# Kernel optimization log

Measured on AMD Instinct MI355X. Metric: run time of the kernel, lower is better.

Reference implementation:

```python
import jax, jax.numpy as jnp
import numpy as np
import math

D, DK, DV = 1024, 128, 128
B, S = 4, 2048

def setup_inputs() -> dict:
    key = jax.random.key(0)
    k1, k2, k3, k4 = jax.random.split(key, 4)
    # xavier_normal std = sqrt(2/(fan_in+fan_out))
    std_qk = math.sqrt(2.0 / (D + DK))
    std_v = math.sqrt(2.0 / (D + DV))
    return {
        "X": jax.random.normal(k1, (B, S, D), dtype=jnp.float32),
        "W_q": jax.random.normal(k2, (D, DK), dtype=jnp.float32) * std_qk,
        "W_k": jax.random.normal(k3, (D, DK), dtype=jnp.float32) * std_qk,
        "W_v": jax.random.normal(k4, (D, DV), dtype=jnp.float32) * std_v,
    }

def reference(X, W_q, W_k, W_v):
    # Q,K,V projections: [B,S,D] @ [D,dk] -> [B,S,dk]
    Q = X @ W_q
    K = X @ W_k
    V = X @ W_v
    scale = 1.0 / math.sqrt(DK)
    # NOTE: original torch code calls A.masked_fill(...) without assigning the
    # result, so the causal mask is never actually applied. We replicate the
    # executed math: unmasked scaled dot-product attention.
    A = jnp.einsum("bqd,bkd->bqk", Q, K) * scale  # [B,S,S]
    A = jax.nn.softmax(A, axis=2)
    return jnp.einsum("bqk,bkv->bqv", A, V)  # [B,S,DV]
```

## Files before the change

kernel.cpp:

```cpp
#include <hip/hip_runtime.h>
#include <stdint.h>
#include <math.h>


typedef __attribute__((ext_vector_type(4))) float  f32x4;
typedef __attribute__((ext_vector_type(4))) short  s16x4;
typedef __attribute__((ext_vector_type(8))) short  s16x8;
typedef __attribute__((ext_vector_type(4))) float  fl4;

#define MFMA16(a,b,c) __builtin_amdgcn_mfma_f32_16x16x16bf16_1k(a,b,c,0,0,0)
#define MFMA32(a,b,c) __builtin_amdgcn_mfma_f32_16x16x32_bf16(a,b,c,0,0,0)

__device__ __forceinline__ short f2bf(float f){
  uint32_t u = __builtin_bit_cast(uint32_t, f);
  u = (u + 0x7FFFu + ((u >> 16) & 1u)) >> 16;
  return (short)u;
}

#define S_LEN   2048
#define D_IN    1024
#define D_HEAD  128
#define NROWS   8192
#define NSPLIT  8
#define KVB     64
#define KVPER   (S_LEN / NSPLIT)
#define NT      (KVPER / KVB)
#define QBLK    64

#define WT_OFF  0u
#define Q_OFF   786432u
#define K_OFF   (786432u + 2097152u)
#define V_OFF   (786432u + 2u*2097152u)
#define OP_OFF  (786432u + 3u*2097152u)
#define ML_OFF  (OP_OFF + 33554432u)

#define LOG2E   1.4426950408889634f
#define DEFER_TH 11.541560327111708f

__global__ __launch_bounds__(256) void wt3_kernel(
    const float* __restrict__ Wq, const float* __restrict__ Wk,
    const float* __restrict__ Wv, short* __restrict__ Wt){
  int i = blockIdx.x * 256 + threadIdx.x;
  int m = i >> 17;
  int r = i & 131071;
  int n = r >> 10;
  int k = r & 1023;
  const float* W = (m == 0) ? Wq : (m == 1 ? Wk : Wv);
  float v = W[k * D_HEAD + n];
  if (m == 0) v *= 0.08838834764831845f * LOG2E;
  Wt[i] = f2bf(v);
}

__global__ __launch_bounds__(256) void proj_kernel(
    const float* __restrict__ X, const short* __restrict__ Wt,
    short* __restrict__ Qo, short* __restrict__ Ko, short* __restrict__ Vt){
  const int mt  = blockIdx.x;
  const int mat = blockIdx.y;
  const short* Wm = Wt + mat * 131072;

  __shared__ short Xs[64][72];
  __shared__ short Ws[128][72];

  const int tid  = threadIdx.x;
  const int lane = tid & 63;
  const int wid  = tid >> 6;
  const int wm   = (wid >> 1) * 32;
  const int wn   = (wid & 1) * 64;
  const int lr   = lane & 15;
  const int lg8  = (lane >> 4) * 8;

  const f32x4 zero4 = {0.f, 0.f, 0.f, 0.f};
  f32x4 acc[2][4];
  #pragma unroll
  for (int mf = 0; mf < 2; mf++)
    #pragma unroll
    for (int n = 0; n < 4; n++) acc[mf][n] = zero4;

  const int xr = tid >> 2, xc = (tid & 3) * 16;
  const int wr = tid >> 1, wc = (tid & 1) * 32;

  const float* xsrc0 = X + (size_t)(mt * 64 + xr) * D_IN + xc;
  const short* wsrc0 = Wm + (size_t)wr * D_IN + wc;

  fl4   xA[4];
  s16x8 wR[4];

  #pragma unroll
  for (int j = 0; j < 4; j++){
    xA[j] = *(const fl4*)(xsrc0 + 4 * j);
    wR[j] = *(const s16x8*)(wsrc0 + 8 * j);
  }

  #pragma unroll 1
  for (int kt = 0; kt < D_IN; kt += 64){
    {
      s16x8 v0, v1;
      #pragma unroll
      for (int j = 0; j < 4; j++){
        v0[j] = f2bf(xA[0][j]); v0[j+4] = f2bf(xA[1][j]);
        v1[j] = f2bf(xA[2][j]); v1[j+4] = f2bf(xA[3][j]);
      }
      *(s16x8*)&Xs[xr][xc]     = v0;
      *(s16x8*)&Xs[xr][xc + 8] = v1;
      #pragma unroll
      for (int j = 0; j < 4; j++) *(s16x8*)&Ws[wr][wc + 8*j] = wR[j];
    }
    __syncthreads();

    if (kt + 64 < D_IN){
      #pragma unroll
      for (int j = 0; j < 4; j++){
        xA[j] = *(const fl4*)(xsrc0 + kt + 64 + 4*j);
        wR[j] = *(const s16x8*)(wsrc0 + kt + 64 + 8*j);
      }
    }

    #pragma unroll
    for (int kc = 0; kc < 64; kc += 32){
      s16x8 af[2];
      #pragma unroll
      for (int mf = 0; mf < 2; mf++)
        af[mf] = *(const s16x8*)&Xs[wm + mf*16 + lr][kc + lg8];
      #pragma unroll
      for (int n = 0; n < 4; n++){
        s16x8 bf = *(const s16x8*)&Ws[wn + n*16 + lr][kc + lg8];
        #pragma unroll
        for (int mf = 0; mf < 2; mf++)
          acc[mf][n] = MFMA32(af[mf], bf, acc[mf][n]);
      }
    }
    __syncthreads();
  }

  const int lg4 = (lane >> 4) * 4;
  if (mat < 2){
    short* dst = (mat == 0) ? Qo : Ko;
    #pragma unroll
    for (int mf = 0; mf < 2; mf++)
      #pragma unroll
      for (int n = 0; n < 4; n++){
        int col = wn + n*16 + lr;
        #pragma unroll
        for (int r = 0; r < 4; r++){
          int row = mt*64 + wm + mf*16 + lg4 + r;
          dst[(size_t)row * D_HEAD + col] = f2bf(acc[mf][n][r]);
        }
      }
  } else {
    const int b  = (mt * 64) >> 11;
    const int s0 = (mt * 64) & 2047;
    #pragma unroll
    for (int mf = 0; mf < 2; mf++)
      #pragma unroll
      for (int n = 0; n < 4; n++){
        int dv = wn + n*16 + lr;
        int s  = s0 + wm + mf*16 + lg4;
        s16x4 v;
        #pragma unroll
        for (int r = 0; r < 4; r++) v[r] = f2bf(acc[mf][n][r]);
        *(s16x4*)&Vt[((size_t)b * D_HEAD + dv) * S_LEN + s] = v;
      }
  }
}

__global__ __launch_bounds__(256, 4) void flash_kernel(
    const short* __restrict__ Q, const short* __restrict__ K,
    const short* __restrict__ Vt, float* __restrict__ Opart,
    float* __restrict__ MLpart){
  const int sp = blockIdx.x;
  const int qt = blockIdx.y;
  const int b  = blockIdx.z;

  __shared__ short Ks[KVB][136];
  __shared__ short Vs[128][72];

  const int tid  = threadIdx.x;
  const int lane = tid & 63;
  const int w    = tid >> 6;
  const int lr   = lane & 15;
  const int lg   = lane >> 4;

  const int qrow = qt * QBLK + w * 16 + lr;
  const short* Qr = Q + (size_t)(b * S_LEN + qrow) * D_HEAD + 8 * lg;
  s16x8 qf[4];
  #pragma unroll
  for (int c = 0; c < 4; c++) qf[c] = *(const s16x8*)(Qr + c * 32);

  const f32x4 zero4 = {0.f, 0.f, 0.f, 0.f};
  f32x4 o[8];
  #pragma unroll
  for (int t = 0; t < 8; t++) o[t] = zero4;
  float m_run = -INFINITY, l_run = 0.0f;

  const short* Kb = K  + (size_t)b * S_LEN * D_HEAD;
  const short* Vb = Vt + (size_t)b * D_HEAD * S_LEN;
  const int kr = tid >> 2, kc = (tid & 3) * 32;
  const int vr = tid >> 1, vc = (tid & 1) * 32;

  s16x8 kR[4], vR[4];
  const int kv_beg = sp * KVPER;

  {
    const short* ks = Kb + (size_t)(kv_beg + kr) * D_HEAD + kc;
    const short* vs = Vb + (size_t)vr * S_LEN + kv_beg + vc;
    #pragma unroll
    for (int j = 0; j < 4; j++){
      kR[j] = *(const s16x8*)(ks + 8*j);
      vR[j] = *(const s16x8*)(vs + 8*j);
    }
  }
  #pragma unroll
  for (int j = 0; j < 4; j++){
    *(s16x8*)&Ks[kr][kc + 8*j] = kR[j];
    *(s16x8*)&Vs[vr][vc + 8*j] = vR[j];
  }
  __syncthreads();

  #pragma unroll 1
  for (int it = 0; it < NT; ++it){
    if (it + 1 < NT){
      int kv0 = kv_beg + (it + 1) * KVB;
      const short* ks = Kb + (size_t)(kv0 + kr) * D_HEAD + kc;
      const short* vs = Vb + (size_t)vr * S_LEN + kv0 + vc;
      #pragma unroll
      for (int j = 0; j < 4; j++){
        kR[j] = *(const s16x8*)(ks + 8*j);
        vR[j] = *(const s16x8*)(vs + 8*j);
      }
    }

    f32x4 sa[4];
    #pragma unroll
    for (int t = 0; t < 4; t++) sa[t] = zero4;
    __builtin_amdgcn_s_setprio(1);
    #pragma unroll
    for (int c = 0; c < 4; c++){
      #pragma unroll
      for (int t = 0; t < 4; t++){
        s16x8 ka = *(const s16x8*)&Ks[t*16 + lr][c*32 + 8*lg];
        sa[t] = MFMA32(ka, qf[c], sa[t]);
      }
    }
    __builtin_amdgcn_s_setprio(0);

    float mx = -INFINITY;
    #pragma unroll
    for (int t = 0; t < 4; t++)
      #pragma unroll
      for (int r = 0; r < 4; r++) mx = fmaxf(mx, sa[t][r]);
    mx = fmaxf(mx, __shfl_xor(mx, 16));
    mx = fmaxf(mx, __shfl_xor(mx, 32));
    if (!__all(mx <= m_run + DEFER_TH)){
      float m_new = fmaxf(m_run, mx);
      float alpha = exp2f(m_run - m_new);
      l_run *= alpha;
      #pragma unroll
      for (int t = 0; t < 8; t++) o[t] *= alpha;
      m_run = m_new;
    }
    s16x4 pb[4];
    float lsum = 0.0f;
    #pragma unroll
    for (int t = 0; t < 4; t++)
      #pragma unroll
      for (int r = 0; r < 4; r++){
        float e = exp2f(sa[t][r] - m_run);
        pb[t][r] = f2bf(e);
        lsum += e;
      }
    lsum += __shfl_xor(lsum, 16);
    lsum += __shfl_xor(lsum, 32);
    l_run += lsum;

    __builtin_amdgcn_s_setprio(1);
    #pragma unroll
    for (int dt = 0; dt < 8; dt++){
      #pragma unroll
      for (int t = 0; t < 4; t++){
        s16x4 va = *(const s16x4*)&Vs[dt*16 + lr][t*16 + 4*lg];
        o[dt] = MFMA16(va, pb[t], o[dt]);
      }
    }
    __builtin_amdgcn_s_setprio(0);

    if (it + 1 < NT){
      __syncthreads();
      #pragma unroll
      for (int j = 0; j < 4; j++){
        *(s16x8*)&Ks[kr][kc + 8*j] = kR[j];
        *(s16x8*)&Vs[vr][vc + 8*j] = vR[j];
      }
      __syncthreads();
    }
  }

  const int lg4 = lg * 4;
  const size_t grow = (size_t)b * S_LEN + qrow;
  float* Op = Opart + ((size_t)sp * NROWS + grow) * D_HEAD + lg4;
  #pragma unroll
  for (int dt = 0; dt < 8; dt++)
    *(f32x4*)(Op + dt * 16) = o[dt];
  if (lg == 0){
    float* ml = MLpart + ((size_t)sp * NROWS + grow) * 2;
    ml[0] = m_run; ml[1] = l_run;
  }
}

__global__ __launch_bounds__(256) void merge_kernel(
    const float* __restrict__ Opart, const float* __restrict__ MLpart,
    float* __restrict__ out){
  int idx = blockIdx.x * 256 + threadIdx.x;
  int row = idx >> 7;
  float m[NSPLIT], l[NSPLIT];
  float M = -INFINITY;
  #pragma unroll
  for (int s = 0; s < NSPLIT; s++){
    m[s] = MLpart[((size_t)s * NROWS + row) * 2 + 0];
    l[s] = MLpart[((size_t)s * NROWS + row) * 2 + 1];
    M = fmaxf(M, m[s]);
  }
  float L = 0.f, val = 0.f;
  #pragma unroll
  for (int s = 0; s < NSPLIT; s++){
    float e = exp2f(m[s] - M);
    L   += l[s] * e;
    val += Opart[(size_t)s * NROWS * D_HEAD + idx] * e;
  }
  out[idx] = val / L;
}

extern "C" void kernel_launch(void* const* d_in, const int* in_sizes, int n_in,
                              void* d_out, int out_size, void* d_ws, size_t ws_size,
                              hipStream_t stream){
  const float* X  = (const float*)d_in[0];
  const float* Wq = (const float*)d_in[1];
  const float* Wk = (const float*)d_in[2];
  const float* Wv = (const float*)d_in[3];
  char* ws = (char*)d_ws;
  short* Wt = (short*)(ws + WT_OFF);
  short* Qp = (short*)(ws + Q_OFF);
  short* Kp = (short*)(ws + K_OFF);
  short* Vt = (short*)(ws + V_OFF);
  float* Op = (float*)(ws + OP_OFF);
  float* Ml = (float*)(ws + ML_OFF);
  float* out = (float*)d_out;

  wt3_kernel  <<<dim3(1536),           dim3(256), 0, stream>>>(Wq, Wk, Wv, Wt);
  proj_kernel <<<dim3(128, 3),         dim3(256), 0, stream>>>(X, Wt, Qp, Kp, Vt);
  flash_kernel<<<dim3(NSPLIT, 32, 4),  dim3(256), 0, stream>>>(Qp, Kp, Vt, Op, Ml);
  merge_kernel<<<dim3(4096),           dim3(256), 0, stream>>>(Op, Ml, out);
}
```

Baseline: 129.0 us.

## Pre-convert X to bf16 and stage projection tiles via direct-to-LDS loads

The weight-transpose kernel now also converts X to bf16 into a workspace buffer, so the projection kernel no longer converts fp32 to bf16 inside its loop. The projection GEMM stages X and W tiles with global_load_lds into double-buffered shared memory using an XOR swizzle instead of padded rows, which overlaps the next tile's load with MFMA work. In exchange, all of X makes an extra round trip through memory (a 32 MB fp32 read and a 16 MB bf16 write) in the pre-pass, and the projection kernel uses more LDS.

```diff
diff --git a/kernel.cpp b/kernel.cpp
--- a/kernel.cpp
+++ b/kernel.cpp
@@ -10,6 +10,12 @@
 
 #define MFMA16(a,b,c) __builtin_amdgcn_mfma_f32_16x16x16bf16_1k(a,b,c,0,0,0)
 #define MFMA32(a,b,c) __builtin_amdgcn_mfma_f32_16x16x32_bf16(a,b,c,0,0,0)
+
+#define AS1 __attribute__((address_space(1)))
+#define AS3 __attribute__((address_space(3)))
+__device__ __forceinline__ void gload16(const void* g, void* l){
+  __builtin_amdgcn_global_load_lds((const AS1 void*)g, (AS3 void*)l, 16, 0, 0);
+}
 
 __device__ __forceinline__ short f2bf(float f){
   uint32_t u = __builtin_bit_cast(uint32_t, f);
@@ -28,38 +34,52 @@
 #define QBLK    64
 
 #define WT_OFF  0u
-#define Q_OFF   786432u
-#define K_OFF   (786432u + 2097152u)
-#define V_OFF   (786432u + 2u*2097152u)
-#define OP_OFF  (786432u + 3u*2097152u)
+#define XB_OFF  786432u
+#define Q_OFF   (786432u + 16777216u)
+#define K_OFF   (Q_OFF + 2097152u)
+#define V_OFF   (K_OFF + 2097152u)
+#define OP_OFF  (V_OFF + 2097152u)
 #define ML_OFF  (OP_OFF + 33554432u)
 
 #define LOG2E   1.4426950408889634f
 #define DEFER_TH 11.541560327111708f
 
-__global__ __launch_bounds__(256) void wt3_kernel(
+__global__ __launch_bounds__(256) void cvt_kernel(
+    const float* __restrict__ X,
     const float* __restrict__ Wq, const float* __restrict__ Wk,
-    const float* __restrict__ Wv, short* __restrict__ Wt){
-  int i = blockIdx.x * 256 + threadIdx.x;
-  int m = i >> 17;
-  int r = i & 131071;
-  int n = r >> 10;
-  int k = r & 1023;
-  const float* W = (m == 0) ? Wq : (m == 1 ? Wk : Wv);
-  float v = W[k * D_HEAD + n];
-  if (m == 0) v *= 0.08838834764831845f * LOG2E;
-  Wt[i] = f2bf(v);
+    const float* __restrict__ Wv, short* __restrict__ Wt,
+    short* __restrict__ Xb){
+  int bid = blockIdx.x;
+  if (bid < 1536){
+    int i = bid * 256 + threadIdx.x;
+    int m = i >> 17;
+    int r = i & 131071;
+    int n = r >> 10;
+    int k = r & 1023;
+    const float* W = (m == 0) ? Wq : (m == 1 ? Wk : Wv);
+    float v = W[k * D_HEAD + n];
+    if (m == 0) v *= 0.08838834764831845f * LOG2E;
+    Wt[i] = f2bf(v);
+  } else {
+    int idx = (bid - 1536) * 256 + threadIdx.x;
+    const fl4* src = (const fl4*)(X + (size_t)idx * 8);
+    fl4 a0 = src[0], a1 = src[1];
+    s16x8 v;
+    #pragma unroll
+    for (int j = 0; j < 4; j++){ v[j] = f2bf(a0[j]); v[j+4] = f2bf(a1[j]); }
+    *(s16x8*)(Xb + (size_t)idx * 8) = v;
+  }
 }
 
 __global__ __launch_bounds__(256) void proj_kernel(
-    const float* __restrict__ X, const short* __restrict__ Wt,
+    const short* __restrict__ Xb, const short* __restrict__ Wt,
     short* __restrict__ Qo, short* __restrict__ Ko, short* __restrict__ Vt){
   const int mt  = blockIdx.x;
   const int mat = blockIdx.y;
   const short* Wm = Wt + mat * 131072;
 
-  __shared__ short Xs[64][72];
-  __shared__ short Ws[128][72];
+  __shared__ short Xs[2][4096];
+  __shared__ short Ws2[2][8192];
 
   const int tid  = threadIdx.x;
   const int lane = tid & 63;
@@ -67,7 +87,8 @@
   const int wm   = (wid >> 1) * 32;
   const int wn   = (wid & 1) * 64;
   const int lr   = lane & 15;
-  const int lg8  = (lane >> 4) * 8;
+  const int lg   = lane >> 4;
+  const int m0   = mt * 64;
 
   const f32x4 zero4 = {0.f, 0.f, 0.f, 0.f};
   f32x4 acc[2][4];
@@ -76,63 +97,59 @@
     #pragma unroll
     for (int n = 0; n < 4; n++) acc[mf][n] = zero4;
 
-  const int xr = tid >> 2, xc = (tid & 3) * 16;
-  const int wr = tid >> 1, wc = (tid & 1) * 32;
-
-  const float* xsrc0 = X + (size_t)(mt * 64 + xr) * D_IN + xc;
-  const short* wsrc0 = Wm + (size_t)wr * D_IN + wc;
-
-  fl4   xA[4];
-  s16x8 wR[4];
-
-  #pragma unroll
-  for (int j = 0; j < 4; j++){
-    xA[j] = *(const fl4*)(xsrc0 + 4 * j);
-    wR[j] = *(const s16x8*)(wsrc0 + 8 * j);
-  }
-
+  #define STAGE(BUFI, KT) do {                                               \
+    _Pragma("unroll")                                                        \
+    for (int c = 0; c < 2; c++){                                             \
+      int off  = wid * 2048 + c * 1024 + lane * 16;                          \
+      int row  = off >> 7;                                                   \
+      int scol = (off & 127) ^ ((row & 7) << 4);                             \
+      const char* g = (const char*)(Xb + (size_t)(m0 + row) * D_IN + (KT))   \
+                      + scol;                                                \
+      gload16(g, (char*)&Xs[BUFI][0] + wid * 2048 + c * 1024);               \
+    }                                                                        \
+    _Pragma("unroll")                                                        \
+    for (int c = 0; c < 4; c++){                                             \
+      int off  = wid * 4096 + c * 1024 + lane * 16;                          \
+      int row  = off >> 7;                                                   \
+      int scol = (off & 127) ^ ((row & 7) << 4);                             \
+      const char* g = (const char*)(Wm + (size_t)row * D_IN + (KT)) + scol;  \
+      gload16(g, (char*)&Ws2[BUFI][0] + wid * 4096 + c * 1024);              \
+    }                                                                        \
+  } while(0)
+
+  STAGE(0, 0);
+  __syncthreads();
+
+  int bufi = 0;
   #pragma unroll 1
   for (int kt = 0; kt < D_IN; kt += 64){
-    {
-      s16x8 v0, v1;
-      #pragma unroll
-      for (int j = 0; j < 4; j++){
-        v0[j] = f2bf(xA[0][j]); v0[j+4] = f2bf(xA[1][j]);
-        v1[j] = f2bf(xA[2][j]); v1[j+4] = f2bf(xA[3][j]);
-      }
-      *(s16x8*)&Xs[xr][xc]     = v0;
-      *(s16x8*)&Xs[xr][xc + 8] = v1;
-      #pragma unroll
-      for (int j = 0; j < 4; j++) *(s16x8*)&Ws[wr][wc + 8*j] = wR[j];
-    }
-    __syncthreads();
-
-    if (kt + 64 < D_IN){
-      #pragma unroll
-      for (int j = 0; j < 4; j++){
-        xA[j] = *(const fl4*)(xsrc0 + kt + 64 + 4*j);
-        wR[j] = *(const s16x8*)(wsrc0 + kt + 64 + 8*j);
-      }
-    }
-
-    #pragma unroll
-    for (int kc = 0; kc < 64; kc += 32){
+    if (kt + 64 < D_IN) STAGE(bufi ^ 1, kt + 64);
+
+    const char* xs = (const char*)&Xs[bufi][0];
+    const char* ws = (const char*)&Ws2[bufi][0];
+    #pragma unroll
+    for (int kc = 0; kc < 2; kc++){
+      const int cb0 = kc * 64 + 16 * lg;
       s16x8 af[2];
       #pragma unroll
-      for (int mf = 0; mf < 2; mf++)
-        af[mf] = *(const s16x8*)&Xs[wm + mf*16 + lr][kc + lg8];
+      for (int mf = 0; mf < 2; mf++){
+        int row = wm + mf*16 + lr;
+        af[mf] = *(const s16x8*)(xs + row*128 + (cb0 ^ ((row & 7) << 4)));
+      }
       #pragma unroll
       for (int n = 0; n < 4; n++){
-        s16x8 bf = *(const s16x8*)&Ws[wn + n*16 + lr][kc + lg8];
+        int row = wn + n*16 + lr;
+        s16x8 bf = *(const s16x8*)(ws + row*128 + (cb0 ^ ((row & 7) << 4)));
         #pragma unroll
         for (int mf = 0; mf < 2; mf++)
           acc[mf][n] = MFMA32(af[mf], bf, acc[mf][n]);
       }
     }
     __syncthreads();
-  }
-
-  const int lg4 = (lane >> 4) * 4;
+    bufi ^= 1;
+  }
+
+  const int lg4 = lg * 4;
   if (mat < 2){
     short* dst = (mat == 0) ? Qo : Ko;
     #pragma unroll
@@ -142,13 +159,13 @@
         int col = wn + n*16 + lr;
         #pragma unroll
         for (int r = 0; r < 4; r++){
-          int row = mt*64 + wm + mf*16 + lg4 + r;
+          int row = m0 + wm + mf*16 + lg4 + r;
           dst[(size_t)row * D_HEAD + col] = f2bf(acc[mf][n][r]);
         }
       }
   } else {
-    const int b  = (mt * 64) >> 11;
-    const int s0 = (mt * 64) & 2047;
+    const int b  = m0 >> 11;
+    const int s0 = m0 & 2047;
     #pragma unroll
     for (int mf = 0; mf < 2; mf++)
       #pragma unroll
@@ -338,6 +355,7 @@
   const float* Wv = (const float*)d_in[3];
   char* ws = (char*)d_ws;
   short* Wt = (short*)(ws + WT_OFF);
+  short* Xb = (short*)(ws + XB_OFF);
   short* Qp = (short*)(ws + Q_OFF);
   short* Kp = (short*)(ws + K_OFF);
   short* Vt = (short*)(ws + V_OFF);
@@ -345,8 +363,8 @@
   float* Ml = (float*)(ws + ML_OFF);
   float* out = (float*)d_out;
 
-  wt3_kernel  <<<dim3(1536),           dim3(256), 0, stream>>>(Wq, Wk, Wv, Wt);
-  proj_kernel <<<dim3(128, 3),         dim3(256), 0, stream>>>(X, Wt, Qp, Kp, Vt);
+  cvt_kernel  <<<dim3(5632),           dim3(256), 0, stream>>>(X, Wq, Wk, Wv, Wt, Xb);
+  proj_kernel <<<dim3(128, 3),         dim3(256), 0, stream>>>(Xb, Wt, Qp, Kp, Vt);
   flash_kernel<<<dim3(NSPLIT, 32, 4),  dim3(256), 0, stream>>>(Qp, Kp, Vt, Op, Ml);
   merge_kernel<<<dim3(4096),           dim3(256), 0, stream>>>(Op, Ml, out);
 }
```

Measured after the change: 131.3 us. About the same (+1.8%).
